# Optimization experiments

Hardware: AMD Instinct MI355X
Metric: run time of the kernel (lower is better)

## Reference

```python
import jax, jax.numpy as jnp
import numpy as np

B, S, H, OUT = 4096, 200, 512, 64


def setup_inputs() -> dict:
    key = jax.random.key(0)
    ks = jax.random.split(key, 16)
    sc = 0.05
    return {
        "last_input": jax.random.normal(ks[0], (B, OUT), jnp.float32),
        "hidden": jax.random.normal(ks[1], (1, B, H), jnp.float32),
        "encoder_outputs": jax.random.normal(ks[2], (S, B, H), jnp.float32),
        "attn_W": jax.random.normal(ks[3], (S, H + OUT), jnp.float32) * sc,
        "attn_b": jax.random.normal(ks[4], (S,), jnp.float32) * sc,
        "comb_W": jax.random.normal(ks[5], (H, H + OUT), jnp.float32) * sc,
        "comb_b": jax.random.normal(ks[6], (H,), jnp.float32) * sc,
        "w_ih": jax.random.normal(ks[7], (3 * H, H), jnp.float32) * sc,
        "w_hh": jax.random.normal(ks[8], (3 * H, H), jnp.float32) * sc,
        "b_ih": jax.random.normal(ks[9], (3 * H,), jnp.float32) * sc,
        "b_hh": jax.random.normal(ks[10], (3 * H,), jnp.float32) * sc,
        "out_W": jax.random.normal(ks[11], (OUT, H), jnp.float32) * sc,
        "out_b": jax.random.normal(ks[12], (OUT,), jnp.float32) * sc,
    }


def reference(last_input, hidden, encoder_outputs, attn_W, attn_b, comb_W,
              comb_b, w_ih, w_hh, b_ih, b_hh, out_W, out_b):
    h0 = hidden[0]  # [B,H]
    # Bahdanau-style attention scores over the encoder sequence
    cat1 = jnp.concatenate([last_input, h0], axis=1)          # [B, OUT+H]
    attn_weights = jax.nn.softmax(cat1 @ attn_W.T + attn_b, axis=1)  # [B,S]
    enc = jnp.transpose(encoder_outputs, (1, 0, 2))            # [B,S,H]
    attn_applied = jnp.einsum('bs,bsh->bh', attn_weights, enc)  # [B,H]
    # combine + relu
    cat2 = jnp.concatenate([last_input, attn_applied], axis=1)  # [B, OUT+H]
    x = jax.nn.relu(cat2 @ comb_W.T + comb_b)                   # [B,H]
    # single-step GRU (PyTorch gate order: r, z, n)
    gi = x @ w_ih.T + b_ih                                      # [B,3H]
    gh = h0 @ w_hh.T + b_hh                                     # [B,3H]
    i_r, i_z, i_n = jnp.split(gi, 3, axis=1)
    h_r, h_z, h_n = jnp.split(gh, 3, axis=1)
    r = jax.nn.sigmoid(i_r + h_r)
    z = jax.nn.sigmoid(i_z + h_z)
    n = jnp.tanh(i_n + r * h_n)
    h_new = (1.0 - z) * n + z * h0                              # [B,H]
    out = h_new @ out_W.T + out_b                               # [B,OUT]
    return out, h_new[None], attn_weights
```

## Files before the change

### kernel.cpp

```cpp
#include <hip/hip_runtime.h>
#include <cstddef>

constexpr int Bn = 4096;
constexpr int Sn = 200;
constexpr int Hn = 512;
constexpr int On = 64;
constexpr int K1 = 576;

constexpr size_t HNEW_OFF = (size_t)Bn * On;
constexpr size_t AW_OFF   = (size_t)Bn * On + (size_t)Bn * Hn;

constexpr size_t CAT1B_OFF = 0;
constexpr size_t CAT2B_OFF = CAT1B_OFF + (size_t)Bn * K1 * 2;
constexpr size_t XB_OFF    = CAT2B_OFF + (size_t)Bn * K1 * 2;
constexpr size_t WIHB_OFF  = XB_OFF    + (size_t)Bn * Hn * 2;
constexpr size_t WHHB_OFF  = WIHB_OFF  + (size_t)3 * Hn * Hn * 2;
constexpr size_t CWB_OFF   = WHHB_OFF  + (size_t)3 * Hn * Hn * 2;
constexpr size_t OWB_OFF   = CWB_OFF   + (size_t)Hn * K1 * 2;
constexpr size_t AWB_OFF   = OWB_OFF   + (size_t)On * Hn * 2;
constexpr size_t LOG_OFF   = AWB_OFF   + (size_t)256 * K1 * 2;
constexpr size_t GIB_OFF   = LOG_OFF   + (size_t)Bn * Sn * 4;
constexpr size_t GHB_OFF   = GIB_OFF   + (size_t)Bn * 3 * Hn * 2;
constexpr size_t HNB_OFF   = GHB_OFF   + (size_t)Bn * 3 * Hn * 2;

typedef __attribute__((ext_vector_type(8))) short bf16x8;
typedef __attribute__((ext_vector_type(4))) float f32x4;

__device__ __forceinline__ float sigmoidf_(float v) { return 1.f / (1.f + __expf(-v)); }
__device__ __forceinline__ unsigned short f2bf(float f) {
    unsigned u = __float_as_uint(f);
    return (unsigned short)((u + 0x7FFFu + ((u >> 16) & 1u)) >> 16);
}
__device__ __forceinline__ float bf2f(unsigned short b) {
    return __uint_as_float((unsigned)b << 16);
}
__device__ __forceinline__ ushort4 pack4(float4 v) {
    ushort4 o = { f2bf(v.x), f2bf(v.y), f2bf(v.z), f2bf(v.w) };
    return o;
}

__global__ __launch_bounds__(256) void cvt_all_kernel(
    const float* __restrict__ hidden, const float* __restrict__ wih,
    const float* __restrict__ whh, const float* __restrict__ combW,
    const float* __restrict__ outW, const float* __restrict__ attnW,
    const float* __restrict__ li,
    unsigned short* __restrict__ cat1b, unsigned short* __restrict__ cat2b,
    unsigned short* __restrict__ wihb, unsigned short* __restrict__ whhb,
    unsigned short* __restrict__ combWb, unsigned short* __restrict__ outWb,
    unsigned short* __restrict__ awWb)
{
    const int blk = blockIdx.x;
    const int t = threadIdx.x;
    if (blk < 2048) {
        size_t off = (size_t)blk * 1024 + (size_t)t * 4;
        int b = (int)(off >> 9), col = (int)(off & 511);
        float4 v = *(const float4*)(hidden + off);
        *(ushort4*)(cat1b + (size_t)b * K1 + On + col) = pack4(v);
    } else if (blk < 3584) {
        size_t off = (size_t)(blk - 2048) * 1024 + (size_t)t * 4;
        const float* s = (blk < 2816) ? wih : whh;
        unsigned short* d = (blk < 2816) ? wihb : whhb;
        if (blk >= 2816) off -= (size_t)768 * 1024;
        float4 v = *(const float4*)(s + off);
        *(ushort4*)(d + off) = pack4(v);
    } else if (blk < 3872) {
        size_t off = (size_t)(blk - 3584) * 1024 + (size_t)t * 4;
        float4 v = *(const float4*)(combW + off);
        *(ushort4*)(combWb + off) = pack4(v);
    } else if (blk < 3904) {
        size_t off = (size_t)(blk - 3872) * 1024 + (size_t)t * 4;
        float4 v = *(const float4*)(outW + off);
        *(ushort4*)(outWb + off) = pack4(v);
    } else if (blk < 4017) {
        size_t off = (size_t)(blk - 3904) * 1024 + (size_t)t * 4;
        if (off < (size_t)Sn * K1) {
            float4 v = *(const float4*)(attnW + off);
            *(ushort4*)(awWb + off) = pack4(v);
        }
    } else if (blk < 4049) {
        size_t off = (size_t)Sn * K1 + (size_t)(blk - 4017) * 1024 + (size_t)t * 4;
        if (off < (size_t)256 * K1) {
            ushort4 z = {0, 0, 0, 0};
            *(ushort4*)(awWb + off) = z;
        }
    } else {
        size_t off = (size_t)(blk - 4049) * 1024 + (size_t)t * 4;
        int b = (int)(off >> 6), col = (int)(off & 63);
        float4 v = *(const float4*)(li + off);
        ushort4 o = pack4(v);
        *(ushort4*)(cat1b + (size_t)b * K1 + col) = o;
        *(ushort4*)(cat2b + (size_t)b * K1 + col) = o;
    }
}

template<int MF, int NF, bool RELU, bool OUT_BF16>
__device__ __forceinline__ void gemm_bt_body(
    const unsigned short* __restrict__ A, int lda,
    const unsigned short* __restrict__ B,
    const float* __restrict__ bias, float* __restrict__ Cf,
    unsigned short* __restrict__ Cb, int K, int ldc,
    int m0, int n0, int nmax)
{
    constexpr int BM = 32 * MF;
    constexpr int BN = 32 * NF;
    __shared__ unsigned short As[BM * 64];
    __shared__ unsigned short Bs[BN * 64];

    const int tid = threadIdx.x;
    const int wave = tid >> 6;
    const int lane = tid & 63;
    const int wm = wave >> 1, wn = wave & 1;
    const int l15 = lane & 15, lg = lane >> 4;

    f32x4 acc[MF][NF];
#pragma unroll
    for (int i = 0; i < MF; ++i)
#pragma unroll
        for (int j = 0; j < NF; ++j) acc[i][j] = (f32x4){0.f, 0.f, 0.f, 0.f};

    for (int kc = 0; kc < K; kc += 64) {
        __syncthreads();
#pragma unroll
        for (int i = 0; i < BM * 8 / 256; ++i) {
            int idx = tid + i * 256;
            int row = idx >> 3, ck = idx & 7;
            uint4 v = *(const uint4*)(A + (size_t)(m0 + row) * lda + kc + ck * 8);
            int byte = row * 128 + ((ck * 16) ^ ((row & 7) << 4));
            *(uint4*)((char*)As + byte) = v;
        }
#pragma unroll
        for (int i = 0; i < BN * 8 / 256; ++i) {
            int idx = tid + i * 256;
            int row = idx >> 3, ck = idx & 7;
            uint4 v = *(const uint4*)(B + (size_t)(n0 + row) * K + kc + ck * 8);
            int byte = row * 128 + ((ck * 16) ^ ((row & 7) << 4));
            *(uint4*)((char*)Bs + byte) = v;
        }
        __syncthreads();
#pragma unroll
        for (int s = 0; s < 2; ++s) {
            bf16x8 af[MF], bfr[NF];
#pragma unroll
            for (int i = 0; i < MF; ++i) {
                int row = wm * (MF * 16) + i * 16 + l15;
                int byte = row * 128 + ((s * 64 + lg * 16) ^ ((row & 7) << 4));
                af[i] = *(const bf16x8*)((const char*)As + byte);
            }
#pragma unroll
            for (int j = 0; j < NF; ++j) {
                int row = wn * (NF * 16) + j * 16 + l15;
                int byte = row * 128 + ((s * 64 + lg * 16) ^ ((row & 7) << 4));
                bfr[j] = *(const bf16x8*)((const char*)Bs + byte);
            }
#pragma unroll
            for (int i = 0; i < MF; ++i)
#pragma unroll
                for (int j = 0; j < NF; ++j)
                    acc[i][j] = __builtin_amdgcn_mfma_f32_16x16x32_bf16(
                        af[i], bfr[j], acc[i][j], 0, 0, 0);
        }
    }

#pragma unroll
    for (int i = 0; i < MF; ++i) {
        int m = m0 + wm * (MF * 16) + i * 16 + lg * 4;
#pragma unroll
        for (int j = 0; j < NF; ++j) {
            int n = n0 + wn * (NF * 16) + j * 16 + l15;
            if (n < nmax) {
                float bv = bias[n];
#pragma unroll
                for (int r = 0; r < 4; ++r) {
                    float v = acc[i][j][r] + bv;
                    if (RELU) v = fmaxf(v, 0.f);
                    if (OUT_BF16) Cb[(size_t)(m + r) * ldc + n] = f2bf(v);
                    else          Cf[(size_t)(m + r) * ldc + n] = v;
                }
            }
        }
    }
}

__global__ __launch_bounds__(256, 2) void scores_gemm_kernel(
    const unsigned short* __restrict__ cat1b, const unsigned short* __restrict__ awWb,
    const float* __restrict__ attn_b, float* __restrict__ logits)
{
    gemm_bt_body<2, 2, false, false>(cat1b, K1, awWb, attn_b, logits, nullptr,
                                     K1, Sn, blockIdx.x * 64, blockIdx.y * 64, Sn);
}

__global__ __launch_bounds__(256, 2) void comb_gemm_kernel(
    const unsigned short* __restrict__ cat2b, const unsigned short* __restrict__ combWb,
    const float* __restrict__ comb_b, unsigned short* __restrict__ xb)
{
    gemm_bt_body<4, 4, true, true>(cat2b, K1, combWb, comb_b, nullptr, xb,
                                   K1, Hn, blockIdx.x * 128, blockIdx.y * 128, Hn);
}

__global__ __launch_bounds__(256, 2) void gates_gemm_kernel(
    const unsigned short* __restrict__ xb, const unsigned short* __restrict__ cat1b,
    const unsigned short* __restrict__ wihb, const unsigned short* __restrict__ whhb,
    const float* __restrict__ b_ih, const float* __restrict__ b_hh,
    unsigned short* __restrict__ gib, unsigned short* __restrict__ ghb)
{
    const int y = blockIdx.y;
    const bool is_gh = (y >= 12);
    const unsigned short* A = is_gh ? (cat1b + On) : xb;
    const int lda = is_gh ? K1 : Hn;
    const unsigned short* B = is_gh ? whhb : wihb;
    const float* bias = is_gh ? b_hh : b_ih;
    unsigned short* C = is_gh ? ghb : gib;
    const int n0 = (is_gh ? y - 12 : y) * 128;
    gemm_bt_body<4, 4, false, true>(A, lda, B, bias, nullptr, C,
                                    Hn, 3 * Hn, blockIdx.x * 128, n0, 3 * Hn);
}

__global__ __launch_bounds__(256, 2) void out_gemm_kernel(
    const unsigned short* __restrict__ hnewb, const unsigned short* __restrict__ outWb,
    const float* __restrict__ out_b, float* __restrict__ dout)
{
    gemm_bt_body<4, 2, false, false>(hnewb, Hn, outWb, out_b, dout, nullptr,
                                     Hn, On, blockIdx.x * 128, 0, On);
}

__global__ __launch_bounds__(256) void softmax_kernel(
    const float* __restrict__ logits, float* __restrict__ dout)
{
    const int row = blockIdx.x * 4 + (threadIdx.x >> 6);
    const int lane = threadIdx.x & 63;
    const float* lp = logits + (size_t)row * Sn;
    float v[4], e[4];
    float m = -3.0e38f;
#pragma unroll
    for (int k = 0; k < 4; ++k) {
        int s = lane + 64 * k;
        v[k] = (s < Sn) ? lp[s] : -3.0e38f;
        m = fmaxf(m, v[k]);
    }
#pragma unroll
    for (int o = 32; o > 0; o >>= 1) m = fmaxf(m, __shfl_xor(m, o, 64));
    float sum = 0.f;
#pragma unroll
    for (int k = 0; k < 4; ++k) {
        int s = lane + 64 * k;
        e[k] = (s < Sn) ? __expf(v[k] - m) : 0.f;
        sum += e[k];
    }
#pragma unroll
    for (int o = 32; o > 0; o >>= 1) sum += __shfl_xor(sum, o, 64);
    float inv = 1.f / sum;
#pragma unroll
    for (int k = 0; k < 4; ++k) {
        int s = lane + 64 * k;
        if (s < Sn) dout[AW_OFF + (size_t)row * Sn + s] = e[k] * inv;
    }
}

__global__ __launch_bounds__(256) void attn_apply_kernel(
    const float* __restrict__ enc, const float* __restrict__ aw,
    unsigned short* __restrict__ cat2b)
{
    __shared__ float wl[8 * Sn];
    const int tid = threadIdx.x;
    const int b0 = blockIdx.x * 8;

    for (int idx = tid; idx < 8 * Sn; idx += 256)
        wl[idx] = aw[(size_t)b0 * Sn + idx];
    __syncthreads();

    const int q = tid >> 7;
    const int hc = tid & 127;
    const f32x4* base = (const f32x4*)enc + ((size_t)(b0 + q * 4)) * 128 + hc;

    f32x4 a0 = {0,0,0,0}, a1 = {0,0,0,0}, a2 = {0,0,0,0}, a3 = {0,0,0,0};

#pragma unroll 2
    for (int s = 0; s < Sn; ++s) {
        const f32x4* p = base + (size_t)s * (Bn * 128);
        f32x4 v0 = __builtin_nontemporal_load(p);
        f32x4 v1 = __builtin_nontemporal_load(p + 128);
        f32x4 v2 = __builtin_nontemporal_load(p + 256);
        f32x4 v3 = __builtin_nontemporal_load(p + 384);
        float w0 = wl[(q * 4 + 0) * Sn + s];
        float w1 = wl[(q * 4 + 1) * Sn + s];
        float w2 = wl[(q * 4 + 2) * Sn + s];
        float w3 = wl[(q * 4 + 3) * Sn + s];
        a0 += v0 * w0; a1 += v1 * w1; a2 += v2 * w2; a3 += v3 * w3;
    }

    const int h = hc * 4;
    f32x4 accs[4] = {a0, a1, a2, a3};
#pragma unroll
    for (int r = 0; r < 4; ++r) {
        ushort4 o = { f2bf(accs[r][0]), f2bf(accs[r][1]), f2bf(accs[r][2]), f2bf(accs[r][3]) };
        *(ushort4*)(cat2b + (size_t)(b0 + q * 4 + r) * K1 + On + h) = o;
    }
}

__global__ __launch_bounds__(256) void gru_elem_kernel(
    const unsigned short* __restrict__ gib, const unsigned short* __restrict__ ghb,
    const float* __restrict__ hidden, float* __restrict__ dout,
    unsigned short* __restrict__ hnewb)
{
    int gid = blockIdx.x * 256 + threadIdx.x;
    int b = gid >> 7;
    int n = (gid & 127) * 4;
    const unsigned short* gi = gib + (size_t)b * (3 * Hn);
    const unsigned short* gh = ghb + (size_t)b * (3 * Hn);
    ushort4 ir = *(const ushort4*)(gi + n);
    ushort4 iz = *(const ushort4*)(gi + Hn + n);
    ushort4 in_ = *(const ushort4*)(gi + 2 * Hn + n);
    ushort4 hr = *(const ushort4*)(gh + n);
    ushort4 hz = *(const ushort4*)(gh + Hn + n);
    ushort4 hn = *(const ushort4*)(gh + 2 * Hn + n);
    float4 h0 = *(const float4*)(hidden + (size_t)b * Hn + n);

    float o[4], irv[4] = {bf2f(ir.x), bf2f(ir.y), bf2f(ir.z), bf2f(ir.w)};
    float izv[4] = {bf2f(iz.x), bf2f(iz.y), bf2f(iz.z), bf2f(iz.w)};
    float inv[4] = {bf2f(in_.x), bf2f(in_.y), bf2f(in_.z), bf2f(in_.w)};
    float hrv[4] = {bf2f(hr.x), bf2f(hr.y), bf2f(hr.z), bf2f(hr.w)};
    float hzv[4] = {bf2f(hz.x), bf2f(hz.y), bf2f(hz.z), bf2f(hz.w)};
    float hnv[4] = {bf2f(hn.x), bf2f(hn.y), bf2f(hn.z), bf2f(hn.w)};
    float h0v[4] = {h0.x, h0.y, h0.z, h0.w};
#pragma unroll
    for (int j = 0; j < 4; ++j) {
        float rg = sigmoidf_(irv[j] + hrv[j]);
        float zg = sigmoidf_(izv[j] + hzv[j]);
        float ng = tanhf(inv[j] + rg * hnv[j]);
        o[j] = (1.f - zg) * ng + zg * h0v[j];
    }
    float4 c = {o[0], o[1], o[2], o[3]};
    *(float4*)&dout[HNEW_OFF + (size_t)b * Hn + n] = c;
    ushort4 ob = { f2bf(o[0]), f2bf(o[1]), f2bf(o[2]), f2bf(o[3]) };
    *(ushort4*)(hnewb + (size_t)b * Hn + n) = ob;
}

extern "C" void kernel_launch(void* const* d_in, const int* in_sizes, int n_in,
                              void* d_out, int out_size, void* d_ws, size_t ws_size,
                              hipStream_t stream)
{
    const float* last_input = (const float*)d_in[0];
    const float* hidden     = (const float*)d_in[1];
    const float* enc        = (const float*)d_in[2];
    const float* attn_W     = (const float*)d_in[3];
    const float* attn_b     = (const float*)d_in[4];
    const float* comb_W     = (const float*)d_in[5];
    const float* comb_b     = (const float*)d_in[6];
    const float* w_ih       = (const float*)d_in[7];
    const float* w_hh       = (const float*)d_in[8];
    const float* b_ih       = (const float*)d_in[9];
    const float* b_hh       = (const float*)d_in[10];
    const float* out_W      = (const float*)d_in[11];
    const float* out_b      = (const float*)d_in[12];

    float* out = (float*)d_out;
    char*  ws  = (char*)d_ws;
    unsigned short* cat1b  = (unsigned short*)(ws + CAT1B_OFF);
    unsigned short* cat2b  = (unsigned short*)(ws + CAT2B_OFF);
    unsigned short* xb     = (unsigned short*)(ws + XB_OFF);
    unsigned short* wihb   = (unsigned short*)(ws + WIHB_OFF);
    unsigned short* whhb   = (unsigned short*)(ws + WHHB_OFF);
    unsigned short* combWb = (unsigned short*)(ws + CWB_OFF);
    unsigned short* outWb  = (unsigned short*)(ws + OWB_OFF);
    unsigned short* awWb   = (unsigned short*)(ws + AWB_OFF);
    float*          logits = (float*)(ws + LOG_OFF);
    unsigned short* gib    = (unsigned short*)(ws + GIB_OFF);
    unsigned short* ghb    = (unsigned short*)(ws + GHB_OFF);
    unsigned short* hnewb  = (unsigned short*)(ws + HNB_OFF);

    cvt_all_kernel<<<4305, 256, 0, stream>>>(hidden, w_ih, w_hh, comb_W, out_W,
                                             attn_W, last_input,
                                             cat1b, cat2b, wihb, whhb, combWb,
                                             outWb, awWb);
    scores_gemm_kernel<<<dim3(Bn / 64, 4), 256, 0, stream>>>(cat1b, awWb, attn_b, logits);
    softmax_kernel<<<Bn / 4, 256, 0, stream>>>(logits, out);
    attn_apply_kernel<<<Bn / 8, 256, 0, stream>>>(enc, out + AW_OFF, cat2b);
    comb_gemm_kernel<<<dim3(Bn / 128, Hn / 128), 256, 0, stream>>>(cat2b, combWb, comb_b, xb);
    gates_gemm_kernel<<<dim3(Bn / 128, 24), 256, 0, stream>>>(xb, cat1b, wihb, whhb,
                                                              b_ih, b_hh, gib, ghb);
    gru_elem_kernel<<<2048, 256, 0, stream>>>(gib, ghb, hidden, out, hnewb);
    out_gemm_kernel<<<Bn / 128, 256, 0, stream>>>(hnewb, outWb, out_b, out);
}
```

Measured before the change: 329.3 us.

## Fuse scores GEMM with softmax and gate GEMMs with GRU elementwise

Merges the attention-score GEMM and the softmax into one kernel that does the row max and sum in registers and LDS, so the fp32 logits buffer is no longer written and read back. Fuses the input and hidden gate GEMMs with the GRU elementwise update, so each block computes the r, z and n gates for a 64x64 tile and applies the nonlinearity directly, removing the bf16 gi/gh round trip and one launch. The attention-apply kernel is also retiled to two batch rows per block for more blocks. The costs are smaller GEMM tiles with a single-buffered K loop and the uncoalesced scalar stores in the GRU epilogue.

```diff
diff --git a/kernel.cpp b/kernel.cpp
--- a/kernel.cpp
+++ b/kernel.cpp
@@ -18,10 +18,7 @@
 constexpr size_t CWB_OFF   = WHHB_OFF  + (size_t)3 * Hn * Hn * 2;
 constexpr size_t OWB_OFF   = CWB_OFF   + (size_t)Hn * K1 * 2;
 constexpr size_t AWB_OFF   = OWB_OFF   + (size_t)On * Hn * 2;
-constexpr size_t LOG_OFF   = AWB_OFF   + (size_t)256 * K1 * 2;
-constexpr size_t GIB_OFF   = LOG_OFF   + (size_t)Bn * Sn * 4;
-constexpr size_t GHB_OFF   = GIB_OFF   + (size_t)Bn * 3 * Hn * 2;
-constexpr size_t HNB_OFF   = GHB_OFF   + (size_t)Bn * 3 * Hn * 2;
+constexpr size_t HNB_OFF   = AWB_OFF   + (size_t)256 * K1 * 2;
 
 typedef __attribute__((ext_vector_type(8))) short bf16x8;
 typedef __attribute__((ext_vector_type(4))) float f32x4;
@@ -30,9 +27,6 @@
 __device__ __forceinline__ unsigned short f2bf(float f) {
     unsigned u = __float_as_uint(f);
     return (unsigned short)((u + 0x7FFFu + ((u >> 16) & 1u)) >> 16);
-}
-__device__ __forceinline__ float bf2f(unsigned short b) {
-    return __uint_as_float((unsigned)b << 16);
 }
 __device__ __forceinline__ ushort4 pack4(float4 v) {
     ushort4 o = { f2bf(v.x), f2bf(v.y), f2bf(v.z), f2bf(v.w) };
@@ -181,14 +175,6 @@
     }
 }
 
-__global__ __launch_bounds__(256, 2) void scores_gemm_kernel(
-    const unsigned short* __restrict__ cat1b, const unsigned short* __restrict__ awWb,
-    const float* __restrict__ attn_b, float* __restrict__ logits)
-{
-    gemm_bt_body<2, 2, false, false>(cat1b, K1, awWb, attn_b, logits, nullptr,
-                                     K1, Sn, blockIdx.x * 64, blockIdx.y * 64, Sn);
-}
-
 __global__ __launch_bounds__(256, 2) void comb_gemm_kernel(
     const unsigned short* __restrict__ cat2b, const unsigned short* __restrict__ combWb,
     const float* __restrict__ comb_b, unsigned short* __restrict__ xb)
@@ -197,142 +183,276 @@
                                    K1, Hn, blockIdx.x * 128, blockIdx.y * 128, Hn);
 }
 
-__global__ __launch_bounds__(256, 2) void gates_gemm_kernel(
+__global__ __launch_bounds__(256, 2) void out_gemm_kernel(
+    const unsigned short* __restrict__ hnewb, const unsigned short* __restrict__ outWb,
+    const float* __restrict__ out_b, float* __restrict__ dout)
+{
+    gemm_bt_body<4, 2, false, false>(hnewb, Hn, outWb, out_b, dout, nullptr,
+                                     Hn, On, blockIdx.x * 128, 0, On);
+}
+
+__global__ __launch_bounds__(256) void scores_softmax_kernel(
+    const unsigned short* __restrict__ cat1b, const unsigned short* __restrict__ awWb,
+    const float* __restrict__ attn_b, float* __restrict__ dout)
+{
+    __shared__ unsigned short As[64 * 64];
+    __shared__ unsigned short Bs[256 * 64];
+    __shared__ float smax[4][64];
+    __shared__ float ssum[4][64];
+
+    const int tid = threadIdx.x;
+    const int m0 = blockIdx.x * 64;
+    const int wave = tid >> 6;
+    const int lane = tid & 63;
+    const int l15 = lane & 15, lg = lane >> 4;
+
+    f32x4 acc[4][4];
+#pragma unroll
+    for (int i = 0; i < 4; ++i)
+#pragma unroll
+        for (int j = 0; j < 4; ++j) acc[i][j] = (f32x4){0.f, 0.f, 0.f, 0.f};
+
+    for (int kc = 0; kc < K1; kc += 64) {
+        __syncthreads();
+#pragma unroll
+        for (int i = 0; i < 2; ++i) {
+            int idx = tid + i * 256;
+            int row = idx >> 3, ck = idx & 7;
+            uint4 v = *(const uint4*)(cat1b + (size_t)(m0 + row) * K1 + kc + ck * 8);
+            int byte = row * 128 + ((ck * 16) ^ ((row & 7) << 4));
+            *(uint4*)((char*)As + byte) = v;
+        }
+#pragma unroll
+        for (int i = 0; i < 8; ++i) {
+            int idx = tid + i * 256;
+            int row = idx >> 3, ck = idx & 7;
+            uint4 v = *(const uint4*)(awWb + (size_t)row * K1 + kc + ck * 8);
+            int byte = row * 128 + ((ck * 16) ^ ((row & 7) << 4));
+            *(uint4*)((char*)Bs + byte) = v;
+        }
+        __syncthreads();
+#pragma unroll
+        for (int s = 0; s < 2; ++s) {
+            bf16x8 af[4], bfr[4];
+#pragma unroll
+            for (int i = 0; i < 4; ++i) {
+                int row = i * 16 + l15;
+                int byte = row * 128 + ((s * 64 + lg * 16) ^ ((row & 7) << 4));
+                af[i] = *(const bf16x8*)((const char*)As + byte);
+            }
+#pragma unroll
+            for (int j = 0; j < 4; ++j) {
+                int row = wave * 64 + j * 16 + l15;
+                int byte = row * 128 + ((s * 64 + lg * 16) ^ ((row & 7) << 4));
+                bfr[j] = *(const bf16x8*)((const char*)Bs + byte);
+            }
+#pragma unroll
+            for (int i = 0; i < 4; ++i)
+#pragma unroll
+                for (int j = 0; j < 4; ++j)
+                    acc[i][j] = __builtin_amdgcn_mfma_f32_16x16x32_bf16(
+                        af[i], bfr[j], acc[i][j], 0, 0, 0);
+        }
+    }
+
+#pragma unroll
+    for (int i = 0; i < 4; ++i)
+#pragma unroll
+        for (int j = 0; j < 4; ++j) {
+            int n = wave * 64 + j * 16 + l15;
+            float bv = (n < Sn) ? attn_b[n] : 0.f;
+#pragma unroll
+            for (int r = 0; r < 4; ++r)
+                acc[i][j][r] = (n < Sn) ? (acc[i][j][r] + bv) : -3.0e38f;
+        }
+
+#pragma unroll
+    for (int i = 0; i < 4; ++i) {
+#pragma unroll
+        for (int r = 0; r < 4; ++r) {
+            float mx = fmaxf(fmaxf(acc[i][0][r], acc[i][1][r]),
+                             fmaxf(acc[i][2][r], acc[i][3][r]));
+#pragma unroll
+            for (int o = 8; o > 0; o >>= 1) mx = fmaxf(mx, __shfl_xor(mx, o, 64));
+            if (l15 == 0) smax[wave][i * 16 + lg * 4 + r] = mx;
+        }
+    }
+    __syncthreads();
+#pragma unroll
+    for (int i = 0; i < 4; ++i) {
+#pragma unroll
+        for (int r = 0; r < 4; ++r) {
+            int row = i * 16 + lg * 4 + r;
+            float mx = fmaxf(fmaxf(smax[0][row], smax[1][row]),
+                             fmaxf(smax[2][row], smax[3][row]));
+            float sum = 0.f;
+#pragma unroll
+            for (int j = 0; j < 4; ++j) {
+                float e = __expf(acc[i][j][r] - mx);
+                acc[i][j][r] = e;
+                sum += e;
+            }
+#pragma unroll
+            for (int o = 8; o > 0; o >>= 1) sum += __shfl_xor(sum, o, 64);
+            if (l15 == 0) ssum[wave][row] = sum;
+        }
+    }
+    __syncthreads();
+#pragma unroll
+    for (int i = 0; i < 4; ++i) {
+#pragma unroll
+        for (int r = 0; r < 4; ++r) {
+            int row = i * 16 + lg * 4 + r;
+            float inv = 1.f / (ssum[0][row] + ssum[1][row] + ssum[2][row] + ssum[3][row]);
+#pragma unroll
+            for (int j = 0; j < 4; ++j) {
+                int n = wave * 64 + j * 16 + l15;
+                if (n < Sn)
+                    dout[AW_OFF + (size_t)(m0 + row) * Sn + n] = acc[i][j][r] * inv;
+            }
+        }
+    }
+}
+
+__global__ __launch_bounds__(256) void attn_apply_kernel(
+    const float* __restrict__ enc, const float* __restrict__ aw,
+    unsigned short* __restrict__ cat2b)
+{
+    __shared__ float wl[2 * Sn];
+    const int tid = threadIdx.x;
+    const int b0 = blockIdx.x * 2;
+
+    for (int idx = tid; idx < 2 * Sn; idx += 256)
+        wl[idx] = aw[(size_t)b0 * Sn + idx];
+    __syncthreads();
+
+    const int r = tid >> 7;
+    const int hc = tid & 127;
+    const f32x4* base = (const f32x4*)enc + ((size_t)(b0 + r)) * 128 + hc;
+    const float* w = &wl[r * Sn];
+
+    f32x4 acc = {0, 0, 0, 0};
+#pragma unroll 4
+    for (int s = 0; s < Sn; ++s) {
+        f32x4 v = __builtin_nontemporal_load(base + (size_t)s * (Bn * 128));
+        acc += v * w[s];
+    }
+
+    ushort4 o = { f2bf(acc[0]), f2bf(acc[1]), f2bf(acc[2]), f2bf(acc[3]) };
+    *(ushort4*)(cat2b + (size_t)(b0 + r) * K1 + On + hc * 4) = o;
+}
+
+__device__ __forceinline__ void gru_gemm_phase(
+    const unsigned short* __restrict__ A, int lda,
+    const unsigned short* __restrict__ W,
+    int m0, int n0, int tid, int wm, int wn, int l15, int lg,
+    unsigned short* As, unsigned short* Bs,
+    f32x4 aR[2][2], f32x4 aZ[2][2], f32x4 aN[2][2])
+{
+    for (int kc = 0; kc < Hn; kc += 64) {
+        __syncthreads();
+#pragma unroll
+        for (int i = 0; i < 2; ++i) {
+            int idx = tid + i * 256;
+            int row = idx >> 3, ck = idx & 7;
+            uint4 v = *(const uint4*)(A + (size_t)(m0 + row) * lda + kc + ck * 8);
+            int byte = row * 128 + ((ck * 16) ^ ((row & 7) << 4));
+            *(uint4*)((char*)As + byte) = v;
+        }
+#pragma unroll
+        for (int g = 0; g < 3; ++g)
+#pragma unroll
+            for (int i = 0; i < 2; ++i) {
+                int idx = tid + i * 256;
+                int row = idx >> 3, ck = idx & 7;
+                uint4 v = *(const uint4*)(W + (size_t)(g * Hn + n0 + row) * Hn + kc + ck * 8);
+                int byte = row * 128 + ((ck * 16) ^ ((row & 7) << 4));
+                *(uint4*)((char*)Bs + g * 8192 + byte) = v;
+            }
+        __syncthreads();
+#pragma unroll
+        for (int s = 0; s < 2; ++s) {
+            bf16x8 af[2], bf0[2], bf1[2], bf2[2];
+#pragma unroll
+            for (int i = 0; i < 2; ++i) {
+                int row = wm * 32 + i * 16 + l15;
+                int byte = row * 128 + ((s * 64 + lg * 16) ^ ((row & 7) << 4));
+                af[i] = *(const bf16x8*)((const char*)As + byte);
+            }
+#pragma unroll
+            for (int j = 0; j < 2; ++j) {
+                int row = wn * 32 + j * 16 + l15;
+                int byte = row * 128 + ((s * 64 + lg * 16) ^ ((row & 7) << 4));
+                bf0[j] = *(const bf16x8*)((const char*)Bs + 0 * 8192 + byte);
+                bf1[j] = *(const bf16x8*)((const char*)Bs + 1 * 8192 + byte);
+                bf2[j] = *(const bf16x8*)((const char*)Bs + 2 * 8192 + byte);
+            }
+#pragma unroll
+            for (int i = 0; i < 2; ++i)
+#pragma unroll
+                for (int j = 0; j < 2; ++j) {
+                    aR[i][j] = __builtin_amdgcn_mfma_f32_16x16x32_bf16(af[i], bf0[j], aR[i][j], 0, 0, 0);
+                    aZ[i][j] = __builtin_amdgcn_mfma_f32_16x16x32_bf16(af[i], bf1[j], aZ[i][j], 0, 0, 0);
+                    aN[i][j] = __builtin_amdgcn_mfma_f32_16x16x32_bf16(af[i], bf2[j], aN[i][j], 0, 0, 0);
+                }
+        }
+    }
+}
+
+__global__ __launch_bounds__(256, 2) void gru_fused_kernel(
     const unsigned short* __restrict__ xb, const unsigned short* __restrict__ cat1b,
     const unsigned short* __restrict__ wihb, const unsigned short* __restrict__ whhb,
     const float* __restrict__ b_ih, const float* __restrict__ b_hh,
-    unsigned short* __restrict__ gib, unsigned short* __restrict__ ghb)
-{
-    const int y = blockIdx.y;
-    const bool is_gh = (y >= 12);
-    const unsigned short* A = is_gh ? (cat1b + On) : xb;
-    const int lda = is_gh ? K1 : Hn;
-    const unsigned short* B = is_gh ? whhb : wihb;
-    const float* bias = is_gh ? b_hh : b_ih;
-    unsigned short* C = is_gh ? ghb : gib;
-    const int n0 = (is_gh ? y - 12 : y) * 128;
-    gemm_bt_body<4, 4, false, true>(A, lda, B, bias, nullptr, C,
-                                    Hn, 3 * Hn, blockIdx.x * 128, n0, 3 * Hn);
-}
-
-__global__ __launch_bounds__(256, 2) void out_gemm_kernel(
-    const unsigned short* __restrict__ hnewb, const unsigned short* __restrict__ outWb,
-    const float* __restrict__ out_b, float* __restrict__ dout)
-{
-    gemm_bt_body<4, 2, false, false>(hnewb, Hn, outWb, out_b, dout, nullptr,
-                                     Hn, On, blockIdx.x * 128, 0, On);
-}
-
-__global__ __launch_bounds__(256) void softmax_kernel(
-    const float* __restrict__ logits, float* __restrict__ dout)
-{
-    const int row = blockIdx.x * 4 + (threadIdx.x >> 6);
-    const int lane = threadIdx.x & 63;
-    const float* lp = logits + (size_t)row * Sn;
-    float v[4], e[4];
-    float m = -3.0e38f;
-#pragma unroll
-    for (int k = 0; k < 4; ++k) {
-        int s = lane + 64 * k;
-        v[k] = (s < Sn) ? lp[s] : -3.0e38f;
-        m = fmaxf(m, v[k]);
-    }
-#pragma unroll
-    for (int o = 32; o > 0; o >>= 1) m = fmaxf(m, __shfl_xor(m, o, 64));
-    float sum = 0.f;
-#pragma unroll
-    for (int k = 0; k < 4; ++k) {
-        int s = lane + 64 * k;
-        e[k] = (s < Sn) ? __expf(v[k] - m) : 0.f;
-        sum += e[k];
-    }
-#pragma unroll
-    for (int o = 32; o > 0; o >>= 1) sum += __shfl_xor(sum, o, 64);
-    float inv = 1.f / sum;
-#pragma unroll
-    for (int k = 0; k < 4; ++k) {
-        int s = lane + 64 * k;
-        if (s < Sn) dout[AW_OFF + (size_t)row * Sn + s] = e[k] * inv;
-    }
-}
-
-__global__ __launch_bounds__(256) void attn_apply_kernel(
-    const float* __restrict__ enc, const float* __restrict__ aw,
-    unsigned short* __restrict__ cat2b)
-{
-    __shared__ float wl[8 * Sn];
+    const float* __restrict__ hidden,
+    float* __restrict__ dout, unsigned short* __restrict__ hnewb)
+{
+    __shared__ unsigned short As[64 * 64];
+    __shared__ unsigned short Bs[3 * 64 * 64];
+
     const int tid = threadIdx.x;
-    const int b0 = blockIdx.x * 8;
-
-    for (int idx = tid; idx < 8 * Sn; idx += 256)
-        wl[idx] = aw[(size_t)b0 * Sn + idx];
-    __syncthreads();
-
-    const int q = tid >> 7;
-    const int hc = tid & 127;
-    const f32x4* base = (const f32x4*)enc + ((size_t)(b0 + q * 4)) * 128 + hc;
-
-    f32x4 a0 = {0,0,0,0}, a1 = {0,0,0,0}, a2 = {0,0,0,0}, a3 = {0,0,0,0};
-
-#pragma unroll 2
-    for (int s = 0; s < Sn; ++s) {
-        const f32x4* p = base + (size_t)s * (Bn * 128);
-        f32x4 v0 = __builtin_nontemporal_load(p);
-        f32x4 v1 = __builtin_nontemporal_load(p + 128);
-        f32x4 v2 = __builtin_nontemporal_load(p + 256);
-        f32x4 v3 = __builtin_nontemporal_load(p + 384);
-        float w0 = wl[(q * 4 + 0) * Sn + s];
-        float w1 = wl[(q * 4 + 1) * Sn + s];
-        float w2 = wl[(q * 4 + 2) * Sn + s];
-        float w3 = wl[(q * 4 + 3) * Sn + s];
-        a0 += v0 * w0; a1 += v1 * w1; a2 += v2 * w2; a3 += v3 * w3;
-    }
-
-    const int h = hc * 4;
-    f32x4 accs[4] = {a0, a1, a2, a3};
-#pragma unroll
-    for (int r = 0; r < 4; ++r) {
-        ushort4 o = { f2bf(accs[r][0]), f2bf(accs[r][1]), f2bf(accs[r][2]), f2bf(accs[r][3]) };
-        *(ushort4*)(cat2b + (size_t)(b0 + q * 4 + r) * K1 + On + h) = o;
-    }
-}
-
-__global__ __launch_bounds__(256) void gru_elem_kernel(
-    const unsigned short* __restrict__ gib, const unsigned short* __restrict__ ghb,
-    const float* __restrict__ hidden, float* __restrict__ dout,
-    unsigned short* __restrict__ hnewb)
-{
-    int gid = blockIdx.x * 256 + threadIdx.x;
-    int b = gid >> 7;
-    int n = (gid & 127) * 4;
-    const unsigned short* gi = gib + (size_t)b * (3 * Hn);
-    const unsigned short* gh = ghb + (size_t)b * (3 * Hn);
-    ushort4 ir = *(const ushort4*)(gi + n);
-    ushort4 iz = *(const ushort4*)(gi + Hn + n);
-    ushort4 in_ = *(const ushort4*)(gi + 2 * Hn + n);
-    ushort4 hr = *(const ushort4*)(gh + n);
-    ushort4 hz = *(const ushort4*)(gh + Hn + n);
-    ushort4 hn = *(const ushort4*)(gh + 2 * Hn + n);
-    float4 h0 = *(const float4*)(hidden + (size_t)b * Hn + n);
-
-    float o[4], irv[4] = {bf2f(ir.x), bf2f(ir.y), bf2f(ir.z), bf2f(ir.w)};
-    float izv[4] = {bf2f(iz.x), bf2f(iz.y), bf2f(iz.z), bf2f(iz.w)};
-    float inv[4] = {bf2f(in_.x), bf2f(in_.y), bf2f(in_.z), bf2f(in_.w)};
-    float hrv[4] = {bf2f(hr.x), bf2f(hr.y), bf2f(hr.z), bf2f(hr.w)};
-    float hzv[4] = {bf2f(hz.x), bf2f(hz.y), bf2f(hz.z), bf2f(hz.w)};
-    float hnv[4] = {bf2f(hn.x), bf2f(hn.y), bf2f(hn.z), bf2f(hn.w)};
-    float h0v[4] = {h0.x, h0.y, h0.z, h0.w};
-#pragma unroll
-    for (int j = 0; j < 4; ++j) {
-        float rg = sigmoidf_(irv[j] + hrv[j]);
-        float zg = sigmoidf_(izv[j] + hzv[j]);
-        float ng = tanhf(inv[j] + rg * hnv[j]);
-        o[j] = (1.f - zg) * ng + zg * h0v[j];
-    }
-    float4 c = {o[0], o[1], o[2], o[3]};
-    *(float4*)&dout[HNEW_OFF + (size_t)b * Hn + n] = c;
-    ushort4 ob = { f2bf(o[0]), f2bf(o[1]), f2bf(o[2]), f2bf(o[3]) };
-    *(ushort4*)(hnewb + (size_t)b * Hn + n) = ob;
+    const int m0 = blockIdx.x * 64;
+    const int n0 = blockIdx.y * 64;
+    const int wave = tid >> 6, lane = tid & 63;
+    const int wm = wave >> 1, wn = wave & 1;
+    const int l15 = lane & 15, lg = lane >> 4;
+
+    f32x4 aR[2][2], aZ[2][2], aN0[2][2], aN1[2][2];
+#pragma unroll
+    for (int i = 0; i < 2; ++i)
+#pragma unroll
+        for (int j = 0; j < 2; ++j) {
+            aR[i][j] = (f32x4){0.f, 0.f, 0.f, 0.f};
+            aZ[i][j] = (f32x4){0.f, 0.f, 0.f, 0.f};
+            aN0[i][j] = (f32x4){0.f, 0.f, 0.f, 0.f};
+            aN1[i][j] = (f32x4){0.f, 0.f, 0.f, 0.f};
+        }
+
+    gru_gemm_phase(xb, Hn, wihb, m0, n0, tid, wm, wn, l15, lg, As, Bs, aR, aZ, aN0);
+    gru_gemm_phase(cat1b + On, K1, whhb, m0, n0, tid, wm, wn, l15, lg, As, Bs, aR, aZ, aN1);
+
+#pragma unroll
+    for (int j = 0; j < 2; ++j) {
+        const int n = n0 + wn * 32 + j * 16 + l15;
+        const float bR = b_ih[n] + b_hh[n];
+        const float bZ = b_ih[Hn + n] + b_hh[Hn + n];
+        const float bI = b_ih[2 * Hn + n];
+        const float bH = b_hh[2 * Hn + n];
+#pragma unroll
+        for (int i = 0; i < 2; ++i) {
+            const int mb = m0 + wm * 32 + i * 16 + lg * 4;
+#pragma unroll
+            for (int r = 0; r < 4; ++r) {
+                const int m = mb + r;
+                float h0 = hidden[(size_t)m * Hn + n];
+                float rg = sigmoidf_(aR[i][j][r] + bR);
+                float zg = sigmoidf_(aZ[i][j][r] + bZ);
+                float ng = tanhf(aN0[i][j][r] + bI + rg * (aN1[i][j][r] + bH));
+                float o = (1.f - zg) * ng + zg * h0;
+                dout[HNEW_OFF + (size_t)m * Hn + n] = o;
+                hnewb[(size_t)m * Hn + n] = f2bf(o);
+            }
+        }
+    }
 }
 
 extern "C" void kernel_launch(void* const* d_in, const int* in_sizes, int n_in,
@@ -363,21 +483,16 @@
     unsigned short* combWb = (unsigned short*)(ws + CWB_OFF);
     unsigned short* outWb  = (unsigned short*)(ws + OWB_OFF);
     unsigned short* awWb   = (unsigned short*)(ws + AWB_OFF);
-    float*          logits = (float*)(ws + LOG_OFF);
-    unsigned short* gib    = (unsigned short*)(ws + GIB_OFF);
-    unsigned short* ghb    = (unsigned short*)(ws + GHB_OFF);
     unsigned short* hnewb  = (unsigned short*)(ws + HNB_OFF);
 
     cvt_all_kernel<<<4305, 256, 0, stream>>>(hidden, w_ih, w_hh, comb_W, out_W,
                                              attn_W, last_input,
                                              cat1b, cat2b, wihb, whhb, combWb,
                                              outWb, awWb);
-    scores_gemm_kernel<<<dim3(Bn / 64, 4), 256, 0, stream>>>(cat1b, awWb, attn_b, logits);
-    softmax_kernel<<<Bn / 4, 256, 0, stream>>>(logits, out);
-    attn_apply_kernel<<<Bn / 8, 256, 0, stream>>>(enc, out + AW_OFF, cat2b);
+    scores_softmax_kernel<<<Bn / 64, 256, 0, stream>>>(cat1b, awWb, attn_b, out);
+    attn_apply_kernel<<<Bn / 2, 256, 0, stream>>>(enc, out + AW_OFF, cat2b);
     comb_gemm_kernel<<<dim3(Bn / 128, Hn / 128), 256, 0, stream>>>(cat2b, combWb, comb_b, xb);
-    gates_gemm_kernel<<<dim3(Bn / 128, 24), 256, 0, stream>>>(xb, cat1b, wihb, whhb,
-                                                              b_ih, b_hh, gib, ghb);
-    gru_elem_kernel<<<2048, 256, 0, stream>>>(gib, ghb, hidden, out, hnewb);
+    gru_fused_kernel<<<dim3(Bn / 64, Hn / 64), 256, 0, stream>>>(
+        xb, cat1b, wihb, whhb, b_ih, b_hh, hidden, out, hnewb);
     out_gemm_kernel<<<Bn / 128, 256, 0, stream>>>(hnewb, outWb, out_b, out);
 }
```

Measured after the change: 374.6 us. 1.14x slower.
